# Performance work log

Hardware: AMD Instinct MI355X
Metric: run time of the kernel (lower is better)

## Reference

```python
import jax, jax.numpy as jnp
import numpy as np

B, L, C, K = 32, 4096, 128, 64


def setup_inputs() -> dict:
    key = jax.random.key(0)
    x = jax.random.normal(key, (B, L, C), dtype=jnp.float32)
    return {"x": x}


def reference(x) -> jnp.ndarray:
    b, l, c = x.shape
    # (B, C, L) -> rfft along time
    x_freq = jnp.fft.rfft(jnp.transpose(x, (0, 2, 1)), axis=-1)  # (B, C, F) complex
    amps = jnp.abs(x_freq)
    f = amps.shape[-1]
    k = min(K, f)
    _, idx = jax.lax.top_k(amps, k)  # (B, C, k)
    bi = jnp.arange(b)[:, None, None]
    ci = jnp.arange(c)[None, :, None]
    mask = jnp.zeros((b, c, f), dtype=bool).at[bi, ci, idx].set(True)
    x_freq_filtered = jnp.where(mask, x_freq, jnp.zeros_like(x_freq))
    x_time = jnp.fft.irfft(x_freq_filtered, n=l, axis=-1)  # (B, C, L)
    return jnp.transpose(x_time, (0, 2, 1))  # (B, L, C)
```

## Files before the change

### kernel.cpp

```cpp
#include <hip/hip_runtime.h>
#include <math.h>

#define NT   256
#define N2   2048
#define NF   4096
#define KTOP 64
#define BB   32
#define LL   4096
#define CC   128
#define PD(i)  ((i) + ((i) >> 5))
#define PDT(i) ((i) + ((i) >> 3))

union USh {
    double2 zc[2112];
    float   keys[2304];
    float2  zci[2112];
};

__global__ __launch_bounds__(NT, 4)
void fourier_topk_kernel(const float* __restrict__ x, float* __restrict__ out) {
    __shared__ USh u;
    __shared__ double2 Tf[144];
    __shared__ double2 Ff[8];
    __shared__ double2 E1s;
    __shared__ float2  T32[288];
    __shared__ float2  G4[4];
    __shared__ unsigned bc_prefix;
    __shared__ int bc_pack;
    __shared__ int eqc[9][4];

    const int tid  = threadIdx.x;
    const int lane = tid & 63;
    const int w    = tid >> 6;

    int d = blockIdx.x;
    int xcd = d & 7, slot = d >> 3;
    int cid = xcd * 32 + (slot >> 4);
    int within = slot & 15;
    int b = cid >> 3;
    int c = ((cid & 7) << 4) + within;

    const float* xp = x + (size_t)b * LL * CC + c;

    if (tid < 128) { double s, cc; sincospi(-(double)tid / 1024.0, &s, &cc); Tf[PDT(tid)] = make_double2(cc, s); }
    if (tid < 8)   { double s, cc; sincospi(-(double)tid / 8.0,    &s, &cc); Ff[tid]      = make_double2(cc, s); }
    if (tid == 8)  { double s, cc; sincospi(-1.0 / 2048.0,         &s, &cc); E1s          = make_double2(cc, s); }
    { float s, cc; sincospif((float)tid / 1024.0f, &s, &cc); T32[PDT(tid)] = make_float2(cc, s); }
    if (tid < 4)   { float s, cc; sincospif((float)tid / 4.0f, &s, &cc); G4[tid] = make_float2(cc, s); }

    #pragma unroll
    for (int i = 0; i < 8; ++i) {
        int m = tid + NT * i;
        float ev = xp[(size_t)(2 * m)     * CC];
        float od = xp[(size_t)(2 * m + 1) * CC];
        u.zc[PD(m)] = make_double2((double)ev, (double)od);
    }
    __syncthreads();

    #pragma unroll
    for (int LH = 10; LH >= 2; LH -= 2) {
        const int h = 1 << LH, q = h >> 1;
        #pragma unroll
        for (int it = 0; it < 2; ++it) {
            int bf  = tid + NT * it;
            int j   = bf & (q - 1);
            int blk = bf >> (LH - 1);
            int a   = (blk << (LH + 1)) + j;
            double2 x0 = u.zc[PD(a)],     x1 = u.zc[PD(a + q)];
            double2 x2 = u.zc[PD(a + h)], x3 = u.zc[PD(a + h + q)];
            int e1 = j << (10 - LH);
            double2 t = Tf[PDT(e1 & 127)];
            double2 f = Ff[e1 >> 7];
            double wc  = t.x * f.x - t.y * f.y, ws  = t.x * f.y + t.y * f.x;
            double w2c = wc * wc - ws * ws,     w2s = 2.0 * wc * ws;
            double u0r = x0.x + x2.x, u0i = x0.y + x2.y;
            double d0r = x0.x - x2.x, d0i = x0.y - x2.y;
            double u1r = x1.x + x3.x, u1i = x1.y + x3.y;
            double d1r = x1.x - x3.x, d1i = x1.y - x3.y;
            double v0r = d0r * wc - d0i * ws,  v0i = d0r * ws + d0i * wc;
            double v1r = d1r * ws + d1i * wc,  v1i = d1i * ws - d1r * wc;
            double s0r = u0r + u1r, s0i = u0i + u1i;
            double e0r = u0r - u1r, e0i = u0i - u1i;
            double s1r = v0r + v1r, s1i = v0i + v1i;
            double e1r = v0r - v1r, e1i = v0i - v1i;
            u.zc[PD(a)]         = make_double2(s0r, s0i);
            u.zc[PD(a + q)]     = make_double2(e0r * w2c - e0i * w2s, e0r * w2s + e0i * w2c);
            u.zc[PD(a + h)]     = make_double2(s1r, s1i);
            u.zc[PD(a + h + q)] = make_double2(e1r * w2c - e1i * w2s, e1r * w2s + e1i * w2c);
        }
        __syncthreads();
    }
    #pragma unroll
    for (int it = 0; it < 4; ++it) {
        int a = 2 * (tid + NT * it);
        double2 x0 = u.zc[PD(a)], x1 = u.zc[PD(a + 1)];
        u.zc[PD(a)]     = make_double2(x0.x + x1.x, x0.y + x1.y);
        u.zc[PD(a + 1)] = make_double2(x0.x - x1.x, x0.y - x1.y);
    }
    __syncthreads();

    unsigned ku[9]; float fxr[9], fxi[9];
    #pragma unroll
    for (int q9 = 0; q9 < 9; ++q9) {
        int k = tid + NT * q9;
        const bool valid = (q9 < 8) || (tid == 0);
        ku[q9] = 0u; fxr[q9] = 0.f; fxi[q9] = 0.f;
        if (valid) {
            int k1 = k & (N2 - 1), k2 = (N2 - k1) & (N2 - 1);
            int pa = __brev((unsigned)k1) >> 21, pb = __brev((unsigned)k2) >> 21;
            double2 A = u.zc[PD(pa)], Bz = u.zc[PD(pb)];
            double Er = 0.5 * (A.x + Bz.x), Ei = 0.5 * (A.y - Bz.y);
            double Or = 0.5 * (A.y + Bz.y), Oi = 0.5 * (Bz.x - A.x);
            double Xr, Xi;
            if (k == N2) { Xr = Er - Or; Xi = 0.0; }
            else {
                int m = k >> 1, r = k & 1;
                double2 t = Tf[PDT(m & 127)], f = Ff[m >> 7];
                double uc = t.x * f.x - t.y * f.y, us = t.x * f.y + t.y * f.x;
                if (r) {
                    double nc = uc * E1s.x - us * E1s.y;
                    us = uc * E1s.y + us * E1s.x; uc = nc;
                }
                Xr = Er + uc * Or - us * Oi;
                Xi = Ei + uc * Oi + us * Or;
            }
            fxr[q9] = (float)Xr; fxi[q9] = (float)Xi;
            float a2 = (float)(Xr * Xr + Xi * Xi);
            ku[q9] = __float_as_uint(a2);
        }
    }
    __syncthreads();

    #pragma unroll
    for (int q9 = 0; q9 < 9; ++q9) u.keys[tid + NT * q9] = __uint_as_float(ku[q9]);
    __syncthreads();

    if (tid < 64) {
        unsigned lk[36];
        #pragma unroll
        for (int i = 0; i < 36; ++i) lk[i] = __float_as_uint(u.keys[tid + 64 * i]);
        unsigned prefix = 0;
        for (int bit = 30; bit >= 0; --bit) {
            unsigned cand = prefix | (1u << bit);
            int cnt = 0;
            #pragma unroll
            for (int i = 0; i < 36; ++i) cnt += (lk[i] >= cand) ? 1 : 0;
            for (int off = 1; off < 64; off <<= 1) cnt += __shfl_xor(cnt, off);
            if (cnt >= KTOP) prefix = cand;
        }
        int cge = 0, cgt = 0;
        #pragma unroll
        for (int i = 0; i < 36; ++i) { cge += (lk[i] >= prefix) ? 1 : 0; cgt += (lk[i] > prefix) ? 1 : 0; }
        int packed = cge | (cgt << 16);
        for (int off = 1; off < 64; off <<= 1) packed += __shfl_xor(packed, off);
        if (tid == 0) { bc_prefix = prefix; bc_pack = packed; }
    }
    __syncthreads();
    const unsigned prefix = bc_prefix;
    const int cge = bc_pack & 0xFFFF, cgt = bc_pack >> 16;

    bool kp[9];
    if (cge == KTOP) {
        #pragma unroll
        for (int q9 = 0; q9 < 9; ++q9) {
            const bool valid = (q9 < 8) || (tid == 0);
            kp[q9] = valid && (ku[q9] >= prefix);
        }
    } else {
        int need_eq = KTOP - cgt;
        int mb[9]; bool eqf[9];
        #pragma unroll
        for (int q9 = 0; q9 < 9; ++q9) {
            const bool valid = (q9 < 8) || (tid == 0);
            bool eq = valid && (ku[q9] == prefix);
            eqf[q9] = eq;
            unsigned long long bal = __ballot(eq);
            if (lane == 0) eqc[q9][w] = __popcll(bal);
            mb[q9] = __popcll(bal & ((1ull << lane) - 1ull));
        }
        __syncthreads();
        int base = 0;
        #pragma unroll
        for (int q9 = 0; q9 < 9; ++q9) {
            const bool valid = (q9 < 8) || (tid == 0);
            int pw = 0;
            #pragma unroll
            for (int ww = 0; ww < 4; ++ww) pw += (ww < w) ? eqc[q9][ww] : 0;
            int rank = base + pw + mb[q9];
            kp[q9] = (valid && ku[q9] > prefix) || (eqf[q9] && rank < need_eq);
            base += eqc[q9][0] + eqc[q9][1] + eqc[q9][2] + eqc[q9][3];
        }
    }
    __syncthreads();

    #pragma unroll
    for (int i = 0; i < 9; ++i) {
        int idx = tid + NT * i;
        if (idx < 2112) u.zci[idx] = make_float2(0.f, 0.f);
    }
    __syncthreads();

    float* zf = (float*)u.zci;
    #pragma unroll
    for (int q9 = 0; q9 < 9; ++q9) {
        if (kp[q9]) {
            int k = tid + NT * q9;
            float a = fxr[q9], bq = fxi[q9];
            float sth, cth; sincospif((float)k * (1.0f / 2048.0f), &sth, &cth);
            float Px = 0.5f * (1.f - sth), Py = 0.5f * cth;
            if (k < N2) {
                int p = PD((int)(__brev((unsigned)k) >> 21));
                atomicAdd(&zf[2 * p],     a * Px - bq * Py);
                atomicAdd(&zf[2 * p + 1], a * Py + bq * Px);
            }
            if (k > 0) {
                int m2 = (N2 - k) & (N2 - 1);
                int p = PD((int)(__brev((unsigned)m2) >> 21));
                float Qx = 1.f - Px, Qy = Py;
                atomicAdd(&zf[2 * p],     a * Qx + bq * Qy);
                atomicAdd(&zf[2 * p + 1], a * Qy - bq * Qx);
            }
        }
    }
    __syncthreads();

    #pragma unroll
    for (int LH = 0; LH <= 8; LH += 2) {
        const int h = 1 << LH;
        #pragma unroll
        for (int it = 0; it < 2; ++it) {
            int bf  = tid + NT * it;
            int j   = bf & (h - 1);
            int blk = bf >> LH;
            int a   = (blk << (LH + 2)) + j;
            float2 x0 = u.zci[PD(a)],         x1 = u.zci[PD(a + h)];
            float2 x2 = u.zci[PD(a + 2 * h)], x3 = u.zci[PD(a + 3 * h)];
            int eB = j << (9 - LH);
            float2 t = T32[PDT(eB & 255)];
            float2 g = G4[eB >> 8];
            float wbc = t.x * g.x - t.y * g.y, wbs = t.x * g.y + t.y * g.x;
            float wac = wbc * wbc - wbs * wbs, was = 2.f * wbc * wbs;
            float vr = x1.x * wac - x1.y * was, vi = x1.x * was + x1.y * wac;
            float y0r = x0.x + vr, y0i = x0.y + vi, y1r = x0.x - vr, y1i = x0.y - vi;
            float ur = x3.x * wac - x3.y * was, ui = x3.x * was + x3.y * wac;
            float y2r = x2.x + ur, y2i = x2.y + ui, y3r = x2.x - ur, y3i = x2.y - ui;
            float b0r = y2r * wbc - y2i * wbs, b0i = y2r * wbs + y2i * wbc;
            float b1r = -(y3r * wbs) - y3i * wbc, b1i = y3r * wbc - y3i * wbs;
            u.zci[PD(a)]         = make_float2(y0r + b0r, y0i + b0i);
            u.zci[PD(a + 2 * h)] = make_float2(y0r - b0r, y0i - b0i);
            u.zci[PD(a + h)]     = make_float2(y1r + b1r, y1i + b1i);
            u.zci[PD(a + 3 * h)] = make_float2(y1r - b1r, y1i - b1i);
        }
        __syncthreads();
    }
    #pragma unroll
    for (int it = 0; it < 4; ++it) {
        int j = tid + NT * it;
        float2 x0 = u.zci[PD(j)], x1 = u.zci[PD(j + 1024)];
        float2 t = T32[PDT(j & 255)];
        float2 g = G4[j >> 8];
        float wc = t.x * g.x - t.y * g.y, ws = t.x * g.y + t.y * g.x;
        float vr = x1.x * wc - x1.y * ws, vi = x1.x * ws + x1.y * wc;
        u.zci[PD(j)]        = make_float2(x0.x + vr, x0.y + vi);
        u.zci[PD(j + 1024)] = make_float2(x0.x - vr, x0.y - vi);
    }
    __syncthreads();

    float* op = out + (size_t)b * LL * CC + c;
    const float inv = 1.0f / 2048.0f;
    #pragma unroll
    for (int i = 0; i < 8; ++i) {
        int m = tid + NT * i;
        float2 z = u.zci[PD(m)];
        op[(size_t)(2 * m)     * CC] = z.x * inv;
        op[(size_t)(2 * m + 1) * CC] = z.y * inv;
    }
}

extern "C" void kernel_launch(void* const* d_in, const int* in_sizes, int n_in,
                              void* d_out, int out_size, void* d_ws, size_t ws_size,
                              hipStream_t stream) {
    (void)in_sizes; (void)n_in; (void)d_ws; (void)ws_size; (void)out_size;
    const float* x = (const float*)d_in[0];
    float* out = (float*)d_out;
    dim3 grid(BB * CC), block(NT);
    hipLaunchKernelGGL(fourier_topk_kernel, grid, block, 0, stream, x, out);
}
```

Measured before the change: 300.7 us.

## Run forward FFT in fp32 and resolve borderline top-k with exact fp64 DFT

The forward FFT moves from double to single precision, which halves the shared memory footprint and drops slow fp64 math. Occupancy hint goes from 4 to 8 blocks. To keep top-k selection correct, bins whose magnitude lies within a small relative band around the threshold get recomputed as direct fp64 DFTs from global memory, then ranked exactly. This adds a rarely taken but costly path, and a risk if more than 48 borderline bins appear.

```diff
diff --git a/kernel.cpp b/kernel.cpp
--- a/kernel.cpp
+++ b/kernel.cpp
@@ -3,31 +3,33 @@
 
 #define NT   256
 #define N2   2048
-#define NF   4096
 #define KTOP 64
 #define BB   32
 #define LL   4096
 #define CC   128
 #define PD(i)  ((i) + ((i) >> 5))
 #define PDT(i) ((i) + ((i) >> 3))
+#define RSQ2 0.70710678118654752f
+#define E1C  0.99999882345170188f
+#define E1S  (-0.00153398018628477f)
 
 union USh {
-    double2 zc[2112];
-    float   keys[2304];
-    float2  zci[2112];
+    float2 zc[2112];
+    float  keys[2304];
 };
 
-__global__ __launch_bounds__(NT, 4)
+__global__ __launch_bounds__(NT, 8)
 void fourier_topk_kernel(const float* __restrict__ x, float* __restrict__ out) {
     __shared__ USh u;
-    __shared__ double2 Tf[144];
-    __shared__ double2 Ff[8];
-    __shared__ double2 E1s;
-    __shared__ float2  T32[288];
-    __shared__ float2  G4[4];
+    __shared__ float2 T256[288];
+    __shared__ float2 G4s[4];
     __shared__ unsigned bc_prefix;
-    __shared__ int bc_pack;
-    __shared__ int eqc[9][4];
+    __shared__ int redL[4];
+    __shared__ int nbL;
+    __shared__ int kbL[48];
+    __shared__ double eampL[48];
+    __shared__ double dredL[8];
+    __shared__ unsigned long long maskL;
 
     const int tid  = threadIdx.x;
     const int lane = tid & 63;
@@ -42,18 +44,14 @@
 
     const float* xp = x + (size_t)b * LL * CC + c;
 
-    if (tid < 128) { double s, cc; sincospi(-(double)tid / 1024.0, &s, &cc); Tf[PDT(tid)] = make_double2(cc, s); }
-    if (tid < 8)   { double s, cc; sincospi(-(double)tid / 8.0,    &s, &cc); Ff[tid]      = make_double2(cc, s); }
-    if (tid == 8)  { double s, cc; sincospi(-1.0 / 2048.0,         &s, &cc); E1s          = make_double2(cc, s); }
-    { float s, cc; sincospif((float)tid / 1024.0f, &s, &cc); T32[PDT(tid)] = make_float2(cc, s); }
-    if (tid < 4)   { float s, cc; sincospif((float)tid / 4.0f, &s, &cc); G4[tid] = make_float2(cc, s); }
+    { float s, cc; sincospif(-(float)tid / 1024.0f, &s, &cc); T256[PDT(tid)] = make_float2(cc, s); }
+    if (tid < 4) { float s, cc; sincospif(-(float)tid / 4.0f, &s, &cc); G4s[tid] = make_float2(cc, s); }
+    if (tid == 0) nbL = 0;
 
     #pragma unroll
     for (int i = 0; i < 8; ++i) {
         int m = tid + NT * i;
-        float ev = xp[(size_t)(2 * m)     * CC];
-        float od = xp[(size_t)(2 * m + 1) * CC];
-        u.zc[PD(m)] = make_double2((double)ev, (double)od);
+        u.zc[PD(m)] = make_float2(xp[(size_t)(2 * m) * CC], xp[(size_t)(2 * m + 1) * CC]);
     }
     __syncthreads();
 
@@ -66,36 +64,37 @@
             int j   = bf & (q - 1);
             int blk = bf >> (LH - 1);
             int a   = (blk << (LH + 1)) + j;
-            double2 x0 = u.zc[PD(a)],     x1 = u.zc[PD(a + q)];
-            double2 x2 = u.zc[PD(a + h)], x3 = u.zc[PD(a + h + q)];
+            float2 x0 = u.zc[PD(a)],     x1 = u.zc[PD(a + q)];
+            float2 x2 = u.zc[PD(a + h)], x3 = u.zc[PD(a + h + q)];
             int e1 = j << (10 - LH);
-            double2 t = Tf[PDT(e1 & 127)];
-            double2 f = Ff[e1 >> 7];
-            double wc  = t.x * f.x - t.y * f.y, ws  = t.x * f.y + t.y * f.x;
-            double w2c = wc * wc - ws * ws,     w2s = 2.0 * wc * ws;
-            double u0r = x0.x + x2.x, u0i = x0.y + x2.y;
-            double d0r = x0.x - x2.x, d0i = x0.y - x2.y;
-            double u1r = x1.x + x3.x, u1i = x1.y + x3.y;
-            double d1r = x1.x - x3.x, d1i = x1.y - x3.y;
-            double v0r = d0r * wc - d0i * ws,  v0i = d0r * ws + d0i * wc;
-            double v1r = d1r * ws + d1i * wc,  v1i = d1i * ws - d1r * wc;
-            double s0r = u0r + u1r, s0i = u0i + u1i;
-            double e0r = u0r - u1r, e0i = u0i - u1i;
-            double s1r = v0r + v1r, s1i = v0i + v1i;
-            double e1r = v0r - v1r, e1i = v0i - v1i;
-            u.zc[PD(a)]         = make_double2(s0r, s0i);
-            u.zc[PD(a + q)]     = make_double2(e0r * w2c - e0i * w2s, e0r * w2s + e0i * w2c);
-            u.zc[PD(a + h)]     = make_double2(s1r, s1i);
-            u.zc[PD(a + h + q)] = make_double2(e1r * w2c - e1i * w2s, e1r * w2s + e1i * w2c);
+            float2 t = T256[PDT(e1 & 255)];
+            float wc, ws;
+            if (e1 >> 8) { wc = (t.x + t.y) * RSQ2; ws = (t.y - t.x) * RSQ2; }
+            else         { wc = t.x; ws = t.y; }
+            float w2c = wc * wc - ws * ws, w2s = 2.f * wc * ws;
+            float u0r = x0.x + x2.x, u0i = x0.y + x2.y;
+            float d0r = x0.x - x2.x, d0i = x0.y - x2.y;
+            float u1r = x1.x + x3.x, u1i = x1.y + x3.y;
+            float d1r = x1.x - x3.x, d1i = x1.y - x3.y;
+            float v0r = d0r * wc - d0i * ws,  v0i = d0r * ws + d0i * wc;
+            float v1r = d1r * ws + d1i * wc,  v1i = d1i * ws - d1r * wc;
+            float s0r = u0r + u1r, s0i = u0i + u1i;
+            float e0r = u0r - u1r, e0i = u0i - u1i;
+            float s1r = v0r + v1r, s1i = v0i + v1i;
+            float e1r = v0r - v1r, e1i = v0i - v1i;
+            u.zc[PD(a)]         = make_float2(s0r, s0i);
+            u.zc[PD(a + q)]     = make_float2(e0r * w2c - e0i * w2s, e0r * w2s + e0i * w2c);
+            u.zc[PD(a + h)]     = make_float2(s1r, s1i);
+            u.zc[PD(a + h + q)] = make_float2(e1r * w2c - e1i * w2s, e1r * w2s + e1i * w2c);
         }
         __syncthreads();
     }
     #pragma unroll
     for (int it = 0; it < 4; ++it) {
         int a = 2 * (tid + NT * it);
-        double2 x0 = u.zc[PD(a)], x1 = u.zc[PD(a + 1)];
-        u.zc[PD(a)]     = make_double2(x0.x + x1.x, x0.y + x1.y);
-        u.zc[PD(a + 1)] = make_double2(x0.x - x1.x, x0.y - x1.y);
+        float2 x0 = u.zc[PD(a)], x1 = u.zc[PD(a + 1)];
+        u.zc[PD(a)]     = make_float2(x0.x + x1.x, x0.y + x1.y);
+        u.zc[PD(a + 1)] = make_float2(x0.x - x1.x, x0.y - x1.y);
     }
     __syncthreads();
 
@@ -108,25 +107,24 @@
         if (valid) {
             int k1 = k & (N2 - 1), k2 = (N2 - k1) & (N2 - 1);
             int pa = __brev((unsigned)k1) >> 21, pb = __brev((unsigned)k2) >> 21;
-            double2 A = u.zc[PD(pa)], Bz = u.zc[PD(pb)];
-            double Er = 0.5 * (A.x + Bz.x), Ei = 0.5 * (A.y - Bz.y);
-            double Or = 0.5 * (A.y + Bz.y), Oi = 0.5 * (Bz.x - A.x);
-            double Xr, Xi;
-            if (k == N2) { Xr = Er - Or; Xi = 0.0; }
+            float2 A = u.zc[PD(pa)], Bz = u.zc[PD(pb)];
+            float Er = 0.5f * (A.x + Bz.x), Ei = 0.5f * (A.y - Bz.y);
+            float Or = 0.5f * (A.y + Bz.y), Oi = 0.5f * (Bz.x - A.x);
+            float Xr, Xi;
+            if (k == N2) { Xr = Er - Or; Xi = 0.f; }
             else {
                 int m = k >> 1, r = k & 1;
-                double2 t = Tf[PDT(m & 127)], f = Ff[m >> 7];
-                double uc = t.x * f.x - t.y * f.y, us = t.x * f.y + t.y * f.x;
+                float2 t = T256[PDT(m & 255)], g = G4s[m >> 8];
+                float uc = t.x * g.x - t.y * g.y, us = t.x * g.y + t.y * g.x;
                 if (r) {
-                    double nc = uc * E1s.x - us * E1s.y;
-                    us = uc * E1s.y + us * E1s.x; uc = nc;
+                    float nc = uc * E1C - us * E1S;
+                    us = uc * E1S + us * E1C; uc = nc;
                 }
                 Xr = Er + uc * Or - us * Oi;
                 Xi = Ei + uc * Oi + us * Or;
             }
-            fxr[q9] = (float)Xr; fxi[q9] = (float)Xi;
-            float a2 = (float)(Xr * Xr + Xi * Xi);
-            ku[q9] = __float_as_uint(a2);
+            fxr[q9] = Xr; fxi[q9] = Xi;
+            ku[q9] = __float_as_uint(Xr * Xr + Xi * Xi);
         }
     }
     __syncthreads();
@@ -148,59 +146,97 @@
             for (int off = 1; off < 64; off <<= 1) cnt += __shfl_xor(cnt, off);
             if (cnt >= KTOP) prefix = cand;
         }
-        int cge = 0, cgt = 0;
-        #pragma unroll
-        for (int i = 0; i < 36; ++i) { cge += (lk[i] >= prefix) ? 1 : 0; cgt += (lk[i] > prefix) ? 1 : 0; }
-        int packed = cge | (cgt << 16);
-        for (int off = 1; off < 64; off <<= 1) packed += __shfl_xor(packed, off);
-        if (tid == 0) { bc_prefix = prefix; bc_pack = packed; }
-    }
-    __syncthreads();
-    const unsigned prefix = bc_prefix;
-    const int cge = bc_pack & 0xFFFF, cgt = bc_pack >> 16;
+        if (tid == 0) bc_prefix = prefix;
+    }
+    __syncthreads();
+
+    const float tf = __uint_as_float(bc_prefix);
+    const float hi = tf * (1.0f + 1e-4f);
+    const float lo = tf * (1.0f - 1e-4f);
+
+    int nsure = 0;
+    int bsl[9]; bool bfl[9];
+    #pragma unroll
+    for (int q9 = 0; q9 < 9; ++q9) {
+        const bool valid = (q9 < 8) || (tid == 0);
+        float a2 = __uint_as_float(ku[q9]);
+        bool su = valid && (a2 > hi);
+        bool bd = valid && !su && (a2 >= lo);
+        nsure += su ? 1 : 0;
+        bfl[q9] = bd; bsl[q9] = 63;
+        if (bd) {
+            int s2 = atomicAdd(&nbL, 1);
+            if (s2 < 48) { kbL[s2] = tid + NT * q9; bsl[q9] = s2; }
+        }
+    }
+    for (int off = 1; off < 64; off <<= 1) nsure += __shfl_xor(nsure, off);
+    if (lane == 0) redL[w] = nsure;
+    __syncthreads();
+    const int n_sure = redL[0] + redL[1] + redL[2] + redL[3];
+    const int need   = KTOP - n_sure;
+    const int nb     = min(nbL, 48);
+
+    unsigned long long selmask;
+    if (nb > need) {
+        for (int i = 0; i < nb; ++i) {
+            int k = kbL[i];
+            double sr = 0.0, si = 0.0;
+            #pragma unroll
+            for (int j = 0; j < 16; ++j) {
+                int t = tid + NT * j;
+                int m = (k * t) & (2 * N2 - 1);
+                double sn, cs; sincospi(-(double)m / 2048.0, &sn, &cs);
+                double xv = (double)xp[(size_t)t * CC];
+                sr = fma(xv, cs, sr); si = fma(xv, sn, si);
+            }
+            for (int off = 1; off < 64; off <<= 1) {
+                sr += __shfl_xor(sr, off); si += __shfl_xor(si, off);
+            }
+            if (lane == 0) { dredL[2 * w] = sr; dredL[2 * w + 1] = si; }
+            __syncthreads();
+            if (tid == 0) {
+                double R = dredL[0] + dredL[2] + dredL[4] + dredL[6];
+                double I = dredL[1] + dredL[3] + dredL[5] + dredL[7];
+                eampL[i] = R * R + I * I;
+            }
+            __syncthreads();
+        }
+        if (tid == 0) {
+            unsigned long long m = 0;
+            for (int s2 = 0; s2 < need; ++s2) {
+                int best = -1, bk = 1 << 30; double bv = -1.0;
+                for (int i = 0; i < nb; ++i) {
+                    if ((m >> i) & 1ull) continue;
+                    double v = eampL[i]; int k = kbL[i];
+                    if (v > bv || (v == bv && k < bk)) { bv = v; bk = k; best = i; }
+                }
+                m |= 1ull << best;
+            }
+            maskL = m;
+        }
+        __syncthreads();
+        selmask = maskL;
+    } else {
+        selmask = ~0ull;
+    }
 
     bool kp[9];
-    if (cge == KTOP) {
-        #pragma unroll
-        for (int q9 = 0; q9 < 9; ++q9) {
-            const bool valid = (q9 < 8) || (tid == 0);
-            kp[q9] = valid && (ku[q9] >= prefix);
-        }
-    } else {
-        int need_eq = KTOP - cgt;
-        int mb[9]; bool eqf[9];
-        #pragma unroll
-        for (int q9 = 0; q9 < 9; ++q9) {
-            const bool valid = (q9 < 8) || (tid == 0);
-            bool eq = valid && (ku[q9] == prefix);
-            eqf[q9] = eq;
-            unsigned long long bal = __ballot(eq);
-            if (lane == 0) eqc[q9][w] = __popcll(bal);
-            mb[q9] = __popcll(bal & ((1ull << lane) - 1ull));
-        }
-        __syncthreads();
-        int base = 0;
-        #pragma unroll
-        for (int q9 = 0; q9 < 9; ++q9) {
-            const bool valid = (q9 < 8) || (tid == 0);
-            int pw = 0;
-            #pragma unroll
-            for (int ww = 0; ww < 4; ++ww) pw += (ww < w) ? eqc[q9][ww] : 0;
-            int rank = base + pw + mb[q9];
-            kp[q9] = (valid && ku[q9] > prefix) || (eqf[q9] && rank < need_eq);
-            base += eqc[q9][0] + eqc[q9][1] + eqc[q9][2] + eqc[q9][3];
-        }
+    #pragma unroll
+    for (int q9 = 0; q9 < 9; ++q9) {
+        const bool valid = (q9 < 8) || (tid == 0);
+        float a2 = __uint_as_float(ku[q9]);
+        kp[q9] = (valid && a2 > hi) || (bfl[q9] && ((selmask >> bsl[q9]) & 1ull));
     }
     __syncthreads();
 
     #pragma unroll
     for (int i = 0; i < 9; ++i) {
         int idx = tid + NT * i;
-        if (idx < 2112) u.zci[idx] = make_float2(0.f, 0.f);
-    }
-    __syncthreads();
-
-    float* zf = (float*)u.zci;
+        if (idx < 2112) u.zc[idx] = make_float2(0.f, 0.f);
+    }
+    __syncthreads();
+
+    float* zf = (float*)u.zc;
     #pragma unroll
     for (int q9 = 0; q9 < 9; ++q9) {
         if (kp[q9]) {
@@ -233,12 +269,14 @@
             int j   = bf & (h - 1);
             int blk = bf >> LH;
             int a   = (blk << (LH + 2)) + j;
-            float2 x0 = u.zci[PD(a)],         x1 = u.zci[PD(a + h)];
-            float2 x2 = u.zci[PD(a + 2 * h)], x3 = u.zci[PD(a + 3 * h)];
+            float2 x0 = u.zc[PD(a)],         x1 = u.zc[PD(a + h)];
+            float2 x2 = u.zc[PD(a + 2 * h)], x3 = u.zc[PD(a + 3 * h)];
             int eB = j << (9 - LH);
-            float2 t = T32[PDT(eB & 255)];
-            float2 g = G4[eB >> 8];
-            float wbc = t.x * g.x - t.y * g.y, wbs = t.x * g.y + t.y * g.x;
+            float2 t = T256[PDT(eB & 255)];
+            float cc, ss;
+            if (eB >> 8) { cc = (t.x + t.y) * RSQ2; ss = (t.y - t.x) * RSQ2; }
+            else         { cc = t.x; ss = t.y; }
+            float wbc = cc, wbs = -ss;
             float wac = wbc * wbc - wbs * wbs, was = 2.f * wbc * wbs;
             float vr = x1.x * wac - x1.y * was, vi = x1.x * was + x1.y * wac;
             float y0r = x0.x + vr, y0i = x0.y + vi, y1r = x0.x - vr, y1i = x0.y - vi;
@@ -246,23 +284,23 @@
             float y2r = x2.x + ur, y2i = x2.y + ui, y3r = x2.x - ur, y3i = x2.y - ui;
             float b0r = y2r * wbc - y2i * wbs, b0i = y2r * wbs + y2i * wbc;
             float b1r = -(y3r * wbs) - y3i * wbc, b1i = y3r * wbc - y3i * wbs;
-            u.zci[PD(a)]         = make_float2(y0r + b0r, y0i + b0i);
-            u.zci[PD(a + 2 * h)] = make_float2(y0r - b0r, y0i - b0i);
-            u.zci[PD(a + h)]     = make_float2(y1r + b1r, y1i + b1i);
-            u.zci[PD(a + 3 * h)] = make_float2(y1r - b1r, y1i - b1i);
+            u.zc[PD(a)]         = make_float2(y0r + b0r, y0i + b0i);
+            u.zc[PD(a + 2 * h)] = make_float2(y0r - b0r, y0i - b0i);
+            u.zc[PD(a + h)]     = make_float2(y1r + b1r, y1i + b1i);
+            u.zc[PD(a + 3 * h)] = make_float2(y1r - b1r, y1i - b1i);
         }
         __syncthreads();
     }
     #pragma unroll
     for (int it = 0; it < 4; ++it) {
         int j = tid + NT * it;
-        float2 x0 = u.zci[PD(j)], x1 = u.zci[PD(j + 1024)];
-        float2 t = T32[PDT(j & 255)];
-        float2 g = G4[j >> 8];
-        float wc = t.x * g.x - t.y * g.y, ws = t.x * g.y + t.y * g.x;
+        float2 x0 = u.zc[PD(j)], x1 = u.zc[PD(j + 1024)];
+        float2 t = T256[PDT(j & 255)], g = G4s[j >> 8];
+        float cc = t.x * g.x - t.y * g.y, ss = t.x * g.y + t.y * g.x;
+        float wc = cc, ws = -ss;
         float vr = x1.x * wc - x1.y * ws, vi = x1.x * ws + x1.y * wc;
-        u.zci[PD(j)]        = make_float2(x0.x + vr, x0.y + vi);
-        u.zci[PD(j + 1024)] = make_float2(x0.x - vr, x0.y - vi);
+        u.zc[PD(j)]        = make_float2(x0.x + vr, x0.y + vi);
+        u.zc[PD(j + 1024)] = make_float2(x0.x - vr, x0.y - vi);
     }
     __syncthreads();
 
@@ -271,7 +309,7 @@
     #pragma unroll
     for (int i = 0; i < 8; ++i) {
         int m = tid + NT * i;
-        float2 z = u.zci[PD(m)];
+        float2 z = u.zc[PD(m)];
         op[(size_t)(2 * m)     * CC] = z.x * inv;
         op[(size_t)(2 * m + 1) * CC] = z.y * inv;
     }
```

Result: slower. 368.3 us (+22.5%).
